# Kernel optimization log

Measured on AMD Instinct MI355X. Metric: run time of the kernel, lower is better.

The kernel has to match this reference:

```python
import jax, jax.numpy as jnp
import numpy as np

B, N, D = 8, 1024, 1024

def setup_inputs() -> dict:
    key = jax.random.key(0)
    k1, k2, k3, k4, k5 = jax.random.split(key, 5)
    x = jax.random.normal(k1, (B, N, D), dtype=jnp.float32)
    y = jax.random.normal(k2, (B, N, D), dtype=jnp.float32)
    adj = jax.random.uniform(k3, (B, N, N), dtype=jnp.float32)
    adj_sumrow = jnp.sum(adj, axis=-1, keepdims=True)  # [B, N, 1], row-sum normalizer
    W = jax.random.normal(k4, (D, D), dtype=jnp.float32) * (1.0 / np.sqrt(D))
    b = jax.random.normal(k5, (D,), dtype=jnp.float32) * 0.02
    return {"x": x, "y": y, "adj": adj, "adj_sumrow": adj_sumrow, "W": W, "b": b}

def reference(x, y, adj, adj_sumrow, W, b):
    # GraphConvolutionCustom: project neighbor features, aggregate via dense adj,
    # normalize by row-sum, add bias and residual input x; then ReLU.
    # Dropout is identity in eval mode (training=False).
    support = jnp.einsum('bnd,de->bne', y, W)          # [B, N, D]
    agg = jnp.matmul(adj, support) / adj_sumrow        # [B, N, D]
    out = jax.nn.relu(agg + b + x)
    return out
```

## Files before the change

### kernel.cpp

```cpp
#include <hip/hip_runtime.h>
#include <hip/hip_bf16.h>
#include <stdint.h>


typedef float  f32x4  __attribute__((ext_vector_type(4)));
typedef __bf16 bf16x8 __attribute__((ext_vector_type(8)));

__device__ __forceinline__ unsigned short f2bf(float f) {
  union { float f; unsigned int u; } c; c.f = f;
  unsigned int u = c.u;
  u += 0x7FFFu + ((u >> 16) & 1u);
  return (unsigned short)(u >> 16);
}

__device__ __forceinline__ void async_cp16(const void* g, void* l) {
  __builtin_amdgcn_global_load_lds(
      (const __attribute__((address_space(1))) unsigned int*)g,
      (__attribute__((address_space(3))) unsigned int*)l, 16, 0, 0);
}

__device__ __forceinline__ void bar() { asm volatile("s_barrier" ::: "memory"); }
#define VMCNT(n) asm volatile("s_waitcnt vmcnt(" #n ")" ::: "memory")


__global__ __launch_bounds__(256) void k_prep(
    const float4* __restrict__ y4, const float4* __restrict__ a4,
    ushort4* __restrict__ yb, ushort4* __restrict__ ab,
    const float* __restrict__ W, unsigned short* __restrict__ Wt)
{
  __shared__ float t[64][65];
  const int bid = blockIdx.x;
  if (bid < 16384) {
    const int i = bid * 256 + threadIdx.x;
    const bool isY = i < 2097152;
    const float4 v = isY ? y4[i] : a4[i - 2097152];
    ushort4 p;
    p.x = f2bf(v.x); p.y = f2bf(v.y); p.z = f2bf(v.z); p.w = f2bf(v.w);
    if (isY) yb[i] = p; else ab[i - 2097152] = p;
  } else {
    const int id = bid - 16384;
    const int n0 = (id & 15) * 64, k0 = (id >> 4) * 64;
    const int tx = threadIdx.x & 63, ty = threadIdx.x >> 6;
#pragma unroll
    for (int r = ty; r < 64; r += 4)
      t[r][tx] = W[(size_t)(k0 + r) * 1024 + n0 + tx];
    __syncthreads();
#pragma unroll
    for (int r = ty; r < 64; r += 4)
      Wt[(size_t)(n0 + r) * 1024 + k0 + tx] = f2bf(t[tx][r]);
  }
}


__device__ __forceinline__ void stageA(
    const unsigned short* __restrict__ A, int sA, int m0, int k0, int c,
    unsigned short* la, int wave, int rg, int colo)
{
#pragma unroll
  for (int s = 0; s < 2; ++s) {
    const int t = wave * 2 + s;
    const int row0 = c * 128 + t * 8;
    async_cp16(A + (size_t)(m0 + row0 + rg) * sA + k0 + colo, la + row0 * 64);
  }
}

__device__ __forceinline__ void stageB(
    const unsigned short* __restrict__ Bt, int sB, int n0, int k0,
    unsigned short* lb, int wave, int rg, int colo)
{
#pragma unroll
  for (int s = 0; s < 2; ++s) {
    const int t = wave * 2 + s;
    const int row0 = t * 8;
    async_cp16(Bt + (size_t)(n0 + row0 + rg) * sB + k0 + colo, lb + row0 * 64);
  }
}

__device__ __forceinline__ void readA(
    const unsigned short* la, bf16x8 af[2][4], int wm, int quad, int l16)
{
#pragma unroll
  for (int h = 0; h < 2; ++h)
#pragma unroll
    for (int i = 0; i < 4; ++i) {
      const int r = wm + i * 16 + l16;
      af[h][i] = *(const bf16x8*)(la + r * 64 + ((h * 4 + quad + r) & 7) * 8);
    }
}

__device__ __forceinline__ void readB(
    const unsigned short* lb, bf16x8 bfr[2][2], int wn, int nh, int quad, int l16)
{
#pragma unroll
  for (int h = 0; h < 2; ++h)
#pragma unroll
    for (int j = 0; j < 2; ++j) {
      const int r = wn + nh * 32 + j * 16 + l16;
      bfr[h][j] = *(const bf16x8*)(lb + r * 64 + ((h * 4 + quad + r) & 7) * 8);
    }
}

__device__ __forceinline__ void phase16(
    bf16x8 af[2][4], bf16x8 bfr[2][2], f32x4 acc[4][4], int nh)
{
  __builtin_amdgcn_s_setprio(1);
#pragma unroll
  for (int h = 0; h < 2; ++h)
#pragma unroll
    for (int i = 0; i < 4; ++i)
#pragma unroll
      for (int j = 0; j < 2; ++j)
        acc[i][nh * 2 + j] = __builtin_amdgcn_mfma_f32_16x16x32_bf16(
            af[h][i], bfr[h][j], acc[i][nh * 2 + j], 0, 0, 0);
  __builtin_amdgcn_s_setprio(0);
}

__device__ __forceinline__ void gemm_3buf(
    const unsigned short* __restrict__ A,  int sA,
    const unsigned short* __restrict__ Bt, int sB,
    int m0, int n0, f32x4 acc[4][4], unsigned short* lsm, int tid)
{
  const int lane = tid & 63, wave = tid >> 6;
  const int wm = (wave >> 1) * 64, wn = (wave & 1) * 64;
  const int quad = lane >> 4, l16 = lane & 15;
  const int rg = lane >> 3;
  const int colo = (((lane & 7) - rg) & 7) * 8;

  unsigned short* cur = lsm;
  unsigned short* nxt = lsm + 24576;
  unsigned short* stg = lsm + 49152;

  bf16x8 af[2][4], bfr[2][2];

  stageA(A, sA, m0, 0, 0, cur, wave, rg, colo);
  stageA(A, sA, m0, 0, 1, cur, wave, rg, colo);
  stageB(Bt, sB, n0, 0, cur + 16384, wave, rg, colo);
  stageA(A, sA, m0, 64, 0, nxt, wave, rg, colo);
  stageA(A, sA, m0, 64, 1, nxt, wave, rg, colo);
  stageB(Bt, sB, n0, 64, nxt + 16384, wave, rg, colo);
  VMCNT(6);
  bar();

#pragma unroll 1
  for (int T = 0; T < 16; ++T) {
    const int nk = (T + 2) * 64;

    if (T < 14) stageA(A, sA, m0, nk, 0, stg, wave, rg, colo);
    readA(cur, af, wm, quad, l16);
    readB(cur + 16384, bfr, wn, 0, quad, l16);
    bar();
    phase16(af, bfr, acc, 0);
    bar();

    if (T < 14) {
      stageA(A, sA, m0, nk, 1, stg, wave, rg, colo);
      stageB(Bt, sB, n0, nk, stg + 16384, wave, rg, colo);
    }
    readB(cur + 16384, bfr, wn, 1, quad, l16);
    if (T < 14)       { VMCNT(6); }
    else if (T == 14) { VMCNT(0); }
    bar();
    phase16(af, bfr, acc, 1);
    bar();

    unsigned short* tmp = cur; cur = nxt; nxt = stg; stg = tmp;
  }
}

__device__ __forceinline__ void zero_acc(f32x4 acc[4][4]) {
#pragma unroll
  for (int i = 0; i < 4; ++i)
#pragma unroll
    for (int j = 0; j < 4; ++j)
#pragma unroll
      for (int r = 0; r < 4; ++r) acc[i][j][r] = 0.0f;
}


__global__ __launch_bounds__(512, 2) void k_gemm1(
    const unsigned short* __restrict__ Wt,
    const unsigned short* __restrict__ Ybf,
    unsigned short* __restrict__ Sup2)
{
  __shared__ __align__(16) unsigned short lsm[73728];
  const int tid = threadIdx.x;
  const int xcd = blockIdx.x & 7, slot = blockIdx.x >> 3;
  const int m0 = (slot >> 3) * 256;
  const int n0 = (xcd * 8 + (slot & 7)) * 128;

  f32x4 acc[4][4];
  zero_acc(acc);
  gemm_3buf(Wt, 1024, Ybf, 1024, m0, n0, acc, lsm, tid);

  const int lane = tid & 63, wave = tid >> 6;
  const int wm = (wave >> 1) * 64, wn = (wave & 1) * 64;
  const int quad = lane >> 4, l16 = lane & 15;
#pragma unroll
  for (int mi = 0; mi < 4; ++mi) {
    const int mb = m0 + wm + mi * 16 + quad * 4;
#pragma unroll
    for (int r = 0; r < 4; ++r) {
      unsigned short* row = Sup2 + ((size_t)(mb + r) << 13);
#pragma unroll
      for (int nj = 0; nj < 4; ++nj)
        row[n0 + wn + nj * 16 + l16] = f2bf(acc[mi][nj][r]);
    }
  }
}


__global__ __launch_bounds__(512, 2) void k_gemm2(
    const unsigned short* __restrict__ AdjBf,
    const unsigned short* __restrict__ Sup2,
    const float* __restrict__ x,
    const float* __restrict__ sumrow,
    const float* __restrict__ bias,
    float* __restrict__ out)
{
  __shared__ __align__(16) unsigned short lsm[73728];
  const int tid = threadIdx.x;
  const int b = blockIdx.x & 7, slot = blockIdx.x >> 3;
  const int m0 = (slot >> 3) * 256, n0 = (slot & 7) * 128;

  f32x4 acc[4][4];
  zero_acc(acc);
  gemm_3buf(AdjBf + ((size_t)b << 20), 1024,
            Sup2 + ((size_t)b << 10), 8192,
            m0, n0, acc, lsm, tid);

  const float* xb = x   + ((size_t)b << 20);
  float*       ob = out + ((size_t)b << 20);
  const float* sr = sumrow + ((size_t)b << 10);
  const int lane = tid & 63, wave = tid >> 6;
  const int wm = (wave >> 1) * 64, wn = (wave & 1) * 64;
  const int quad = lane >> 4, l16 = lane & 15;

  float bv[4];
#pragma unroll
  for (int nj = 0; nj < 4; ++nj) bv[nj] = bias[n0 + wn + nj * 16 + l16];

#pragma unroll
  for (int mi = 0; mi < 4; ++mi) {
    const int mb = m0 + wm + mi * 16 + quad * 4;
#pragma unroll
    for (int r = 0; r < 4; ++r) {
      const int m = mb + r;
      const float inv = 1.0f / sr[m];
#pragma unroll
      for (int nj = 0; nj < 4; ++nj) {
        const int n = n0 + wn + nj * 16 + l16;
        const size_t idx = (((size_t)m) << 10) + n;
        float v = acc[mi][nj][r] * inv + bv[nj] + xb[idx];
        ob[idx] = fmaxf(v, 0.0f);
      }
    }
  }
}


extern "C" void kernel_launch(void* const* d_in, const int* in_sizes, int n_in,
                              void* d_out, int out_size, void* d_ws, size_t ws_size,
                              hipStream_t stream) {
  const float* x      = (const float*)d_in[0];
  const float* y      = (const float*)d_in[1];
  const float* adj    = (const float*)d_in[2];
  const float* sumrow = (const float*)d_in[3];
  const float* W      = (const float*)d_in[4];
  const float* bias   = (const float*)d_in[5];
  float* out = (float*)d_out;

  char* ws = (char*)d_ws;
  unsigned short* ybf   = (unsigned short*)(ws);
  unsigned short* adjbf = (unsigned short*)(ws + ((size_t)16 << 20));
  unsigned short* wt    = (unsigned short*)(ws + ((size_t)32 << 20));
  unsigned short* sup2  = (unsigned short*)(ws + ((size_t)34 << 20));

  k_prep<<<dim3(16640), dim3(256), 0, stream>>>(
      (const float4*)y, (const float4*)adj, (ushort4*)ybf, (ushort4*)adjbf, W, wt);
  k_gemm1<<<dim3(256), dim3(512), 0, stream>>>(wt, ybf, sup2);
  k_gemm2<<<dim3(256), dim3(512), 0, stream>>>(adjbf, sup2, x, sumrow, bias, out);
}
```

Baseline: 200.7 us.

## Rebalance GEMM async staging per phase and coarsen bf16 conversion kernel

The A and B tile staging is reordered so that each half-iteration issues an equal share of the async global-to-LDS copies, with B split into two 32-row halves and A rows interleaved by 64-row wave group. The second phase now reloads the A fragments from LDS, which adds LDS read traffic in exchange for possibly lower register pressure. The prep kernel now converts 8 float4 elements per thread over 2048 blocks instead of one per thread over 16384 blocks, cutting block launch and scheduling overhead. The transpose shared buffer is scoped to its branch.

Result: no change. 203.5 us (+1.4%).

```diff
diff --git a/kernel.cpp b/kernel.cpp
--- a/kernel.cpp
+++ b/kernel.cpp
@@ -28,17 +28,22 @@
     ushort4* __restrict__ yb, ushort4* __restrict__ ab,
     const float* __restrict__ W, unsigned short* __restrict__ Wt)
 {
-  __shared__ float t[64][65];
   const int bid = blockIdx.x;
-  if (bid < 16384) {
-    const int i = bid * 256 + threadIdx.x;
-    const bool isY = i < 2097152;
-    const float4 v = isY ? y4[i] : a4[i - 2097152];
-    ushort4 p;
-    p.x = f2bf(v.x); p.y = f2bf(v.y); p.z = f2bf(v.z); p.w = f2bf(v.w);
-    if (isY) yb[i] = p; else ab[i - 2097152] = p;
+  if (bid < 2048) {
+    const bool isY = bid < 1024;
+    const float4* __restrict__ src = isY ? y4 : a4;
+    ushort4* __restrict__ dst = isY ? yb : ab;
+    int idx = (bid & 1023) * 256 + (int)threadIdx.x;
+#pragma unroll
+    for (int it = 0; it < 8; ++it, idx += 262144) {
+      const float4 v = src[idx];
+      ushort4 p;
+      p.x = f2bf(v.x); p.y = f2bf(v.y); p.z = f2bf(v.z); p.w = f2bf(v.w);
+      dst[idx] = p;
+    }
   } else {
-    const int id = bid - 16384;
+    __shared__ float t[64][65];
+    const int id = bid - 2048;
     const int n0 = (id & 15) * 64, k0 = (id >> 4) * 64;
     const int tx = threadIdx.x & 63, ty = threadIdx.x >> 6;
 #pragma unroll
@@ -52,28 +57,24 @@
 }
 
 
-__device__ __forceinline__ void stageA(
+__device__ __forceinline__ void stageA_u(
     const unsigned short* __restrict__ A, int sA, int m0, int k0, int c,
     unsigned short* la, int wave, int rg, int colo)
 {
 #pragma unroll
   for (int s = 0; s < 2; ++s) {
     const int t = wave * 2 + s;
-    const int row0 = c * 128 + t * 8;
+    const int row0 = (t >> 2) * 64 + c * 32 + (t & 3) * 8;
     async_cp16(A + (size_t)(m0 + row0 + rg) * sA + k0 + colo, la + row0 * 64);
   }
 }
 
-__device__ __forceinline__ void stageB(
-    const unsigned short* __restrict__ Bt, int sB, int n0, int k0,
+__device__ __forceinline__ void stageB_u(
+    const unsigned short* __restrict__ Bt, int sB, int n0, int k0, int u,
     unsigned short* lb, int wave, int rg, int colo)
 {
-#pragma unroll
-  for (int s = 0; s < 2; ++s) {
-    const int t = wave * 2 + s;
-    const int row0 = t * 8;
-    async_cp16(Bt + (size_t)(n0 + row0 + rg) * sB + k0 + colo, lb + row0 * 64);
-  }
+  const int row0 = u * 32 + (wave & 3) * 8 + (wave >> 2) * 64;
+  async_cp16(Bt + (size_t)(n0 + row0 + rg) * sB + k0 + colo, lb + row0 * 64);
 }
 
 __device__ __forceinline__ void readA(
@@ -88,20 +89,20 @@
     }
 }
 
-__device__ __forceinline__ void readB(
-    const unsigned short* lb, bf16x8 bfr[2][2], int wn, int nh, int quad, int l16)
+__device__ __forceinline__ void readBh(
+    const unsigned short* lb, bf16x8 bfr[2][2], int wn, int half, int quad, int l16)
 {
 #pragma unroll
   for (int h = 0; h < 2; ++h)
 #pragma unroll
     for (int j = 0; j < 2; ++j) {
-      const int r = wn + nh * 32 + j * 16 + l16;
+      const int r = wn + half * 32 + j * 16 + l16;
       bfr[h][j] = *(const bf16x8*)(lb + r * 64 + ((h * 4 + quad + r) & 7) * 8);
     }
 }
 
-__device__ __forceinline__ void phase16(
-    bf16x8 af[2][4], bf16x8 bfr[2][2], f32x4 acc[4][4], int nh)
+__device__ __forceinline__ void mfma16(
+    bf16x8 af[2][4], bf16x8 bfr[2][2], f32x4 acc[4][4], int half)
 {
   __builtin_amdgcn_s_setprio(1);
 #pragma unroll
@@ -110,12 +111,12 @@
     for (int i = 0; i < 4; ++i)
 #pragma unroll
       for (int j = 0; j < 2; ++j)
-        acc[i][nh * 2 + j] = __builtin_amdgcn_mfma_f32_16x16x32_bf16(
-            af[h][i], bfr[h][j], acc[i][nh * 2 + j], 0, 0, 0);
+        acc[i][half * 2 + j] = __builtin_amdgcn_mfma_f32_16x16x32_bf16(
+            af[h][i], bfr[h][j], acc[i][half * 2 + j], 0, 0, 0);
   __builtin_amdgcn_s_setprio(0);
 }
 
-__device__ __forceinline__ void gemm_3buf(
+__device__ __forceinline__ void gemm_fine(
     const unsigned short* __restrict__ A,  int sA,
     const unsigned short* __restrict__ Bt, int sB,
     int m0, int n0, f32x4 acc[4][4], unsigned short* lsm, int tid)
@@ -126,44 +127,54 @@
   const int rg = lane >> 3;
   const int colo = (((lane & 7) - rg) & 7) * 8;
 
-  unsigned short* cur = lsm;
-  unsigned short* nxt = lsm + 24576;
-  unsigned short* stg = lsm + 49152;
-
   bf16x8 af[2][4], bfr[2][2];
 
-  stageA(A, sA, m0, 0, 0, cur, wave, rg, colo);
-  stageA(A, sA, m0, 0, 1, cur, wave, rg, colo);
-  stageB(Bt, sB, n0, 0, cur + 16384, wave, rg, colo);
-  stageA(A, sA, m0, 64, 0, nxt, wave, rg, colo);
-  stageA(A, sA, m0, 64, 1, nxt, wave, rg, colo);
-  stageB(Bt, sB, n0, 64, nxt + 16384, wave, rg, colo);
-  VMCNT(6);
-  bar();
-
+  {
+    unsigned short* b0 = lsm;
+    unsigned short* b1 = lsm + 24576;
+    stageA_u(A, sA, m0, 0, 0, b0, wave, rg, colo);
+    stageA_u(A, sA, m0, 0, 1, b0, wave, rg, colo);
+    stageB_u(Bt, sB, n0, 0, 0, b0 + 16384, wave, rg, colo);
+    stageB_u(Bt, sB, n0, 0, 1, b0 + 16384, wave, rg, colo);
+    stageA_u(A, sA, m0, 64, 0, b1, wave, rg, colo);
+    stageA_u(A, sA, m0, 64, 1, b1, wave, rg, colo);
+    stageB_u(Bt, sB, n0, 64, 0, b1 + 16384, wave, rg, colo);
+    stageB_u(Bt, sB, n0, 64, 1, b1 + 16384, wave, rg, colo);
+    VMCNT(6);
+    bar();
+  }
+
+  int curi = 0, stgi = 2;
 #pragma unroll 1
   for (int T = 0; T < 16; ++T) {
+    const unsigned short* cur = lsm + curi * 24576;
+    unsigned short* stg = lsm + stgi * 24576;
     const int nk = (T + 2) * 64;
 
-    if (T < 14) stageA(A, sA, m0, nk, 0, stg, wave, rg, colo);
+    if (T < 14) {
+      stageA_u(A, sA, m0, nk, 0, stg, wave, rg, colo);
+      stageB_u(Bt, sB, n0, nk, 0, stg + 16384, wave, rg, colo);
+    }
     readA(cur, af, wm, quad, l16);
-    readB(cur + 16384, bfr, wn, 0, quad, l16);
-    bar();
-    phase16(af, bfr, acc, 0);
+    readBh(cur + 16384, bfr, wn, 0, quad, l16);
+    bar();
+    mfma16(af, bfr, acc, 0);
     bar();
 
     if (T < 14) {
-      stageA(A, sA, m0, nk, 1, stg, wave, rg, colo);
-      stageB(Bt, sB, n0, nk, stg + 16384, wave, rg, colo);
-    }
-    readB(cur + 16384, bfr, wn, 1, quad, l16);
+      stageA_u(A, sA, m0, nk, 1, stg, wave, rg, colo);
+      stageB_u(Bt, sB, n0, nk, 1, stg + 16384, wave, rg, colo);
+    }
+    readA(cur, af, wm, quad, l16);
+    readBh(cur + 16384, bfr, wn, 1, quad, l16);
     if (T < 14)       { VMCNT(6); }
     else if (T == 14) { VMCNT(0); }
     bar();
-    phase16(af, bfr, acc, 1);
-    bar();
-
-    unsigned short* tmp = cur; cur = nxt; nxt = stg; stg = tmp;
+    mfma16(af, bfr, acc, 1);
+    bar();
+
+    curi = (curi + 1) == 3 ? 0 : curi + 1;
+    stgi = (stgi + 1) == 3 ? 0 : stgi + 1;
   }
 }
 
@@ -190,7 +201,7 @@
 
   f32x4 acc[4][4];
   zero_acc(acc);
-  gemm_3buf(Wt, 1024, Ybf, 1024, m0, n0, acc, lsm, tid);
+  gemm_fine(Wt, 1024, Ybf, 1024, m0, n0, acc, lsm, tid);
 
   const int lane = tid & 63, wave = tid >> 6;
   const int wm = (wave >> 1) * 64, wn = (wave & 1) * 64;
@@ -224,7 +235,7 @@
 
   f32x4 acc[4][4];
   zero_acc(acc);
-  gemm_3buf(AdjBf + ((size_t)b << 20), 1024,
+  gemm_fine(AdjBf + ((size_t)b << 20), 1024,
             Sup2 + ((size_t)b << 10), 8192,
             m0, n0, acc, lsm, tid);
 
@@ -275,7 +286,7 @@
   unsigned short* wt    = (unsigned short*)(ws + ((size_t)32 << 20));
   unsigned short* sup2  = (unsigned short*)(ws + ((size_t)34 << 20));
 
-  k_prep<<<dim3(16640), dim3(256), 0, stream>>>(
+  k_prep<<<dim3(2304), dim3(256), 0, stream>>>(
       (const float4*)y, (const float4*)adj, (ushort4*)ybf, (ushort4*)adjbf, W, wt);
   k_gemm1<<<dim3(256), dim3(512), 0, stream>>>(wt, ybf, sup2);
   k_gemm2<<<dim3(256), dim3(512), 0, stream>>>(adjbf, sup2, x, sumrow, bias, out);
```
